# Kernel optimization log

Hardware: AMD Instinct MI355X
Metric: run time of the kernel (lower is better)

Reference implementation:

```python
import jax, jax.numpy as jnp
import numpy as np
import math

B, H, N, D = 8, 8, 2048, 64
CLIP = 10.0
NEG_INF = 1.0e10

def setup_inputs() -> dict:
    key = jax.random.key(0)
    kq, kk, kv, km = jax.random.split(key, 4)
    Q = jax.random.normal(kq, (B, H, N, D), dtype=jnp.float32)
    K = jax.random.normal(kk, (B, H, N, D), dtype=jnp.float32)
    V = jax.random.normal(kv, (B, H, N, D), dtype=jnp.float32)
    mask = jax.random.randint(km, (B, N, 1), 0, 2).astype(jnp.bool_)
    return {"Q": Q, "K": K, "V": V, "mask": mask}

def reference(Q, K, V, mask):
    scale = math.sqrt(Q.shape[-1])
    # logits: (B, H, Nq, Nk)
    logits = jnp.einsum("bhqd,bhkd->bhqk", Q, K) / scale
    logits = CLIP * jnp.tanh(logits)
    # mask (B, N, 1) -> broadcast over heads and query dim along key axis
    m = mask[:, None, None, :, 0]  # (B, 1, 1, Nk)
    logits = jnp.where(m, -NEG_INF, logits)
    probs = jax.nn.softmax(logits, axis=-1)
    return jnp.einsum("bhqk,bhkd->bhqd", probs, V)
```

## Files before the change

kernel.cpp:

```cpp
#include <hip/hip_runtime.h>

typedef __attribute__((ext_vector_type(8))) short short8;
typedef __attribute__((ext_vector_type(8))) _Float16 half8;
typedef __attribute__((ext_vector_type(2))) __fp16 fp16x2;
typedef __attribute__((ext_vector_type(2))) unsigned int uint2v;
typedef __attribute__((ext_vector_type(16))) float f32x16;
typedef __attribute__((ext_vector_type(4))) float f32x4;
typedef __attribute__((ext_vector_type(8))) unsigned short u16x8;
typedef unsigned int u32;
typedef unsigned short u16;

#define B_ 8
#define H_ 8
#define N_ 2048
#define D_ 64
#define PSTR 72
#define ELEMS 8388608
#define WS_NEED ((48ull << 20) + 4096ull)

static __device__ inline u16 bfhi(float x) {
  u32 u = __float_as_uint(x);
  return (u16)((u + 0x7FFFu + ((u >> 16) & 1u)) >> 16);
}
static __device__ inline float bf2f(u16 h) { return __uint_as_float((u32)h << 16); }
static __device__ inline u16 h2u(_Float16 h) { union { _Float16 f; u16 u; } c; c.f = h; return c.u; }

static __device__ __forceinline__ u32 pkrtz_u32(float a, float b) {
  union { fp16x2 h; u32 u; } c;
  c.h = __builtin_amdgcn_cvt_pkrtz(a, b);
  return c.u;
}

template <bool TAIL>
static __device__ __forceinline__ float pnum(float s, int key, int rem) {
  float z  = __builtin_amdgcn_exp2f(fabsf(s) * -0.36067376022224087f);
  float nu = (s >= 0.f) ? z : 1.f;
  float e  = nu * __builtin_amdgcn_rcpf(1.f + z) * -28.853900817779268f;
  if (TAIL) e = (key < rem) ? e : -16384.f;
  return __builtin_amdgcn_exp2f(e);
}

static __device__ __forceinline__ half8 pack_frag(
    float qa, float qb, float qc, float qd,
    float qe, float qf, float qg, float qh) {
  u32 E0 = pkrtz_u32(qa, qb);
  u32 E1 = pkrtz_u32(qc, qd);
  u32 O0 = pkrtz_u32(qe, qf);
  u32 O1 = pkrtz_u32(qg, qh);
  uint2v w0 = __builtin_amdgcn_permlane32_swap(E0, O0, false, false);
  uint2v w1 = __builtin_amdgcn_permlane32_swap(E1, O1, false, false);
  union { u32 u[4]; half8 v; } c;
  c.u[0] = w0[0]; c.u[1] = w1[0]; c.u[2] = w0[1]; c.u[3] = w1[1];
  return c.v;
}

struct PAFrags { half8 f0, f1, f2, f3; };

#define PN_(S, r, off) pnum<TAIL>(S[r], ((r) & 3) + 8 * ((r) >> 2) + (off), rem)
template <bool TAIL>
static __device__ __forceinline__ PAFrags softmax_repack(
    f32x16 S0, f32x16 S1, int rem) {
  PAFrags o;
  o.f0 = pack_frag(PN_(S0, 0, 0),  PN_(S0, 1, 0),  PN_(S0, 2, 0),  PN_(S0, 3, 0),
                   PN_(S0, 4, 0),  PN_(S0, 5, 0),  PN_(S0, 6, 0),  PN_(S0, 7, 0));
  o.f1 = pack_frag(PN_(S0, 8, 0),  PN_(S0, 9, 0),  PN_(S0, 10, 0), PN_(S0, 11, 0),
                   PN_(S0, 12, 0), PN_(S0, 13, 0), PN_(S0, 14, 0), PN_(S0, 15, 0));
  o.f2 = pack_frag(PN_(S1, 0, 32), PN_(S1, 1, 32), PN_(S1, 2, 32), PN_(S1, 3, 32),
                   PN_(S1, 4, 32), PN_(S1, 5, 32), PN_(S1, 6, 32), PN_(S1, 7, 32));
  o.f3 = pack_frag(PN_(S1, 8, 32), PN_(S1, 9, 32), PN_(S1, 10, 32), PN_(S1, 11, 32),
                   PN_(S1, 12, 32), PN_(S1, 13, 32), PN_(S1, 14, 32), PN_(S1, 15, 32));
  return o;
}

__global__ __launch_bounds__(256) void conv_kv2(
    const float* __restrict__ K, const float* __restrict__ V,
    const int* __restrict__ maskg,
    u16* __restrict__ Khi, u16* __restrict__ Klo, u16* __restrict__ VThi,
    int* __restrict__ cnt) {
  const int kt = blockIdx.x, bh = blockIdx.y, b = bh >> 3, tid = threadIdx.x;
  const int lane = tid & 63, wv = tid >> 6;
  __shared__ float sT[64 * 68];
  __shared__ int sIdx[64];
  __shared__ int wsum[4];
  const int n0 = tid * 8;
  u32 bits = 0; int c = 0;
#pragma unroll
  for (int i = 0; i < 8; ++i)
    if (maskg[b * N_ + n0 + i] == 0) { bits |= (1u << i); ++c; }
  int inc = c;
#pragma unroll
  for (int off = 1; off < 64; off <<= 1) {
    int v = __shfl_up(inc, off);
    if (lane >= off) inc += v;
  }
  if (lane == 63) wsum[wv] = inc;
  if (tid < 64) sIdx[tid] = -1;
  __syncthreads();
  const int cntb = wsum[0] + wsum[1] + wsum[2] + wsum[3];
  int o = inc - c;
#pragma unroll
  for (int k2 = 0; k2 < 4; ++k2) if (k2 < wv) o += wsum[k2];
  const int k0 = kt * 64;
#pragma unroll
  for (int i = 0; i < 8; ++i)
    if (bits & (1u << i)) {
      if (o >= k0 && o < k0 + 64) sIdx[o - k0] = n0 + i;
      ++o;
    }
  if (kt == 0 && (bh & 7) == 0 && tid == 0) cnt[b] = cntb;
  __syncthreads();
  const int nt = (cntb + 63) >> 6;
  if (kt >= nt) return;

  const size_t ibh = (size_t)bh * N_ * D_;
  const size_t okb = ibh + (size_t)kt * 64 * D_;
#pragma unroll
  for (int cc = 0; cc < 2; ++cc) {
    const int ci = tid + cc * 256, row = ci >> 3, seg = ci & 7;
    const int n = sIdx[row];
    f32x4 a, b2, va, vb2;
    if (n >= 0) {
      const float* kp = K + ibh + (size_t)n * D_ + seg * 8;
      a  = *(const f32x4*)kp;
      b2 = *(const f32x4*)(kp + 4);
      const float* vp = V + ibh + (size_t)n * D_ + seg * 8;
      va  = *(const f32x4*)vp;
      vb2 = *(const f32x4*)(vp + 4);
    } else {
#pragma unroll
      for (int j = 0; j < 4; ++j) { a[j] = 0.f; b2[j] = 0.f; va[j] = 0.f; vb2[j] = 0.f; }
    }
    u16x8 h, l;
#pragma unroll
    for (int j = 0; j < 4; ++j) {
      _Float16 h0 = (_Float16)a[j];
      h[j] = h2u(h0); l[j] = h2u((_Float16)(a[j] - (float)h0));
      _Float16 h1 = (_Float16)b2[j];
      h[j + 4] = h2u(h1); l[j + 4] = h2u((_Float16)(b2[j] - (float)h1));
    }
    *(u16x8*)&Khi[okb + row * D_ + seg * 8] = h;
    *(u16x8*)&Klo[okb + row * D_ + seg * 8] = l;
    *(f32x4*)&sT[row * 68 + seg * 8]     = va;
    *(f32x4*)&sT[row * 68 + seg * 8 + 4] = vb2;
  }
  __syncthreads();
  const int d = tid >> 2, ks = tid & 3;
  u16x8 h0, h1;
#pragma unroll
  for (int i = 0; i < 8; ++i) {
    h0[i] = h2u((_Float16)sT[(ks * 16 + i) * 68 + d]);
    h1[i] = h2u((_Float16)sT[(ks * 16 + i + 8) * 68 + d]);
  }
  const size_t ob = (size_t)bh * D_ * N_ + (size_t)d * N_ + (size_t)kt * 64 + ks * 16;
  *(u16x8*)&VThi[ob] = h0; *(u16x8*)&VThi[ob + 8] = h1;
}

__global__ __launch_bounds__(256, 4) void attn_mfma5(
    const float* __restrict__ Qg,
    const u16* __restrict__ Khi, const u16* __restrict__ Klo,
    const u16* __restrict__ VThi,
    const int* __restrict__ cnt, float* __restrict__ Og)
{
  const int qtile = blockIdx.x;
  const int bh = blockIdx.y, b = bh >> 3;
  const int tid = threadIdx.x, w = tid >> 6, lane = tid & 63;
  const int l32 = lane & 31, hl = lane >> 5;
  const int cntb = cnt[b];
  const int nt = (cntb + 63) >> 6;
  const bool partial = (cntb & 63) != 0;

  __shared__ short sKh[64 * PSTR], sKl[64 * PSTR];
  __shared__ short sVh[64 * PSTR];

  half8 qfh[4], qfl[4];
  {
    const float* qp = Qg + ((size_t)bh * N_ + qtile * 128 + w * 32 + l32) * D_ + hl * 8;
#pragma unroll
    for (int s = 0; s < 4; ++s) {
      f32x4 a = *(const f32x4*)(qp + s * 16);
      f32x4 c = *(const f32x4*)(qp + s * 16 + 4);
#pragma unroll
      for (int j = 0; j < 4; ++j) {
        _Float16 h0 = (_Float16)a[j];
        qfh[s][j] = h0; qfl[s][j] = (_Float16)(a[j] - (float)h0);
        _Float16 h1 = (_Float16)c[j];
        qfh[s][j + 4] = h1; qfl[s][j + 4] = (_Float16)(c[j] - (float)h1);
      }
    }
  }
  half8 ones;
#pragma unroll
  for (int j = 0; j < 8; ++j) ones[j] = (l32 == 0) ? (_Float16)1.f : (_Float16)0.f;

  f32x16 accO0, accO1, accD;
#pragma unroll
  for (int i = 0; i < 16; ++i) { accO0[i] = 0.f; accO1[i] = 0.f; accD[i] = 0.f; }

  const size_t kvb = (size_t)bh * N_ * D_;

  for (int kt = 0; kt < nt; ++kt) {
    const int k0 = kt * 64;
    __syncthreads();

#pragma unroll
    for (int cc = 0; cc < 2; ++cc) {
      const int ci = tid + cc * 256, row = ci >> 3, seg = ci & 7;
      const int lofs = row * PSTR + seg * 8;
      const size_t kofs = kvb + (size_t)(k0 + row) * D_ + seg * 8;
      *(short8*)&sKh[lofs] = *(const short8*)&Khi[kofs];
      *(short8*)&sKl[lofs] = *(const short8*)&Klo[kofs];
      const size_t vofs = kvb + (size_t)row * N_ + k0 + seg * 8;
      *(short8*)&sVh[lofs] = *(const short8*)&VThi[vofs];
    }
    __syncthreads();

    f32x16 S0, S1;
#pragma unroll
    for (int i = 0; i < 16; ++i) { S0[i] = 0.f; S1[i] = 0.f; }
    __builtin_amdgcn_s_setprio(1);
#pragma unroll
    for (int s = 0; s < 4; ++s) {
      const int o0 = l32 * PSTR + s * 16 + hl * 8;
      half8 kfh = *(const half8*)&sKh[o0];
      half8 kfl = *(const half8*)&sKl[o0];
      S0 = __builtin_amdgcn_mfma_f32_32x32x16_f16(kfh, qfh[s], S0, 0, 0, 0);
      S0 = __builtin_amdgcn_mfma_f32_32x32x16_f16(kfl, qfh[s], S0, 0, 0, 0);
      S0 = __builtin_amdgcn_mfma_f32_32x32x16_f16(kfh, qfl[s], S0, 0, 0, 0);
      const int o1 = (32 + l32) * PSTR + s * 16 + hl * 8;
      half8 kgh = *(const half8*)&sKh[o1];
      half8 kgl = *(const half8*)&sKl[o1];
      S1 = __builtin_amdgcn_mfma_f32_32x32x16_f16(kgh, qfh[s], S1, 0, 0, 0);
      S1 = __builtin_amdgcn_mfma_f32_32x32x16_f16(kgl, qfh[s], S1, 0, 0, 0);
      S1 = __builtin_amdgcn_mfma_f32_32x32x16_f16(kgh, qfl[s], S1, 0, 0, 0);
    }
    __builtin_amdgcn_s_setprio(0);

    PAFrags pa;
    if (partial && kt == nt - 1)
      pa = softmax_repack<true>(S0, S1, cntb - k0 - 4 * hl);
    else
      pa = softmax_repack<false>(S0, S1, 0);

    __builtin_amdgcn_s_setprio(1);
#pragma unroll
    for (int s = 0; s < 4; ++s) {
      half8 pf = (s == 0) ? pa.f0 : (s == 1) ? pa.f1 : (s == 2) ? pa.f2 : pa.f3;
      const int o0 = l32 * PSTR + s * 16 + hl * 8;
      half8 v0 = *(const half8*)&sVh[o0];
      accO0 = __builtin_amdgcn_mfma_f32_32x32x16_f16(pf, v0, accO0, 0, 0, 0);
      const int o1 = (32 + l32) * PSTR + s * 16 + hl * 8;
      half8 v1 = *(const half8*)&sVh[o1];
      accO1 = __builtin_amdgcn_mfma_f32_32x32x16_f16(pf, v1, accO1, 0, 0, 0);
      accD  = __builtin_amdgcn_mfma_f32_32x32x16_f16(pf, ones, accD, 0, 0, 0);
    }
    __builtin_amdgcn_s_setprio(0);
  }

  const size_t obase = (size_t)bh * N_ + qtile * 128 + w * 32;
#pragma unroll
  for (int r = 0; r < 16; ++r) {
    float den = __shfl(accD[r], lane & 32);
    float inv = (den > 0.f) ? (1.f / den) : 0.f;
    const int row = (r & 3) + 8 * (r >> 2) + 4 * hl;
    Og[(obase + row) * D_ + l32]      = accO0[r] * inv;
    Og[(obase + row) * D_ + 32 + l32] = accO1[r] * inv;
  }
}

__global__ __launch_bounds__(256, 3) void attn_mfma(
    const float* __restrict__ Qg, const float* __restrict__ Kg,
    const float* __restrict__ Vg, const int* __restrict__ maskg,
    float* __restrict__ Og)
{
  const int qtile = blockIdx.x;
  const int bh    = blockIdx.y;
  const int b     = bh >> 3;
  const int tid   = threadIdx.x;
  const int w     = tid >> 6;
  const int lane  = tid & 63;
  const int l32   = lane & 31;
  const int hl    = lane >> 5;
  const int qh    = w >> 1;
  const int kh    = w & 1;

  __shared__ short sKh[64 * PSTR], sKl[64 * PSTR];
  __shared__ short sVh[64 * PSTR], sVl[64 * PSTR];
  __shared__ short sP [64 * PSTR];
  __shared__ float sM[64];

  short8 qfh[4], qfl[4];
  {
    const float* qp = Qg + ((size_t)bh * N_ + qtile * 64 + qh * 32 + l32) * D_ + hl * 8;
#pragma unroll
    for (int s = 0; s < 4; ++s) {
      f32x4 a = *(const f32x4*)(qp + s * 16);
      f32x4 c = *(const f32x4*)(qp + s * 16 + 4);
#pragma unroll
      for (int j = 0; j < 4; ++j) {
        u16 h0 = bfhi(a[j]);
        qfh[s][j] = (short)h0;
        qfl[s][j] = (short)bfhi(a[j] - bf2f(h0));
        u16 h1 = bfhi(c[j]);
        qfh[s][j + 4] = (short)h1;
        qfl[s][j + 4] = (short)bfhi(c[j] - bf2f(h1));
      }
    }
  }
  short8 ones;
#pragma unroll
  for (int j = 0; j < 8; ++j) ones[j] = (short)((l32 == 0) ? 0x3F80 : 0);
  f32x16 accO, accD;
#pragma unroll
  for (int i = 0; i < 16; ++i) { accO[i] = 0.f; accD[i] = 0.f; }
  const size_t kvbase = (size_t)bh * N_ * D_;

  for (int kt = 0; kt < N_ / 64; ++kt) {
    const int k0 = kt * 64;
    __syncthreads();
    {
      const int row = tid >> 2, seg = tid & 3;
      const float* kp = Kg + kvbase + (size_t)(k0 + row) * D_ + seg * 16;
      short8 h0, h1, l0, l1;
#pragma unroll
      for (int i2 = 0; i2 < 2; ++i2) {
        f32x4 t0 = *(const f32x4*)(kp + i2 * 8);
        f32x4 t1 = *(const f32x4*)(kp + i2 * 8 + 4);
#pragma unroll
        for (int j = 0; j < 4; ++j) {
          u16 ha = bfhi(t0[j]); u16 la = bfhi(t0[j] - bf2f(ha));
          u16 hb = bfhi(t1[j]); u16 lb = bfhi(t1[j] - bf2f(hb));
          if (i2 == 0) { h0[j]=(short)ha; l0[j]=(short)la; h0[j+4]=(short)hb; l0[j+4]=(short)lb; }
          else         { h1[j]=(short)ha; l1[j]=(short)la; h1[j+4]=(short)hb; l1[j+4]=(short)lb; }
        }
      }
      *(short8*)&sKh[row * PSTR + seg * 16]     = h0;
      *(short8*)&sKh[row * PSTR + seg * 16 + 8] = h1;
      *(short8*)&sKl[row * PSTR + seg * 16]     = l0;
      *(short8*)&sKl[row * PSTR + seg * 16 + 8] = l1;
    }
    {
      const float* vp = Vg + kvbase + (size_t)(k0 + w * 16) * D_ + lane;
      float vv[16];
#pragma unroll
      for (int kk = 0; kk < 16; ++kk) vv[kk] = vp[(size_t)kk * D_];
      short8 h0, h1, l0, l1;
#pragma unroll
      for (int kk = 0; kk < 8; ++kk) {
        u16 ha = bfhi(vv[kk]);     h0[kk]=(short)ha; l0[kk]=(short)bfhi(vv[kk]-bf2f(ha));
        u16 hb = bfhi(vv[kk + 8]); h1[kk]=(short)hb; l1[kk]=(short)bfhi(vv[kk+8]-bf2f(hb));
      }
      *(short8*)&sVh[lane * PSTR + w * 16]     = h0;
      *(short8*)&sVh[lane * PSTR + w * 16 + 8] = h1;
      *(short8*)&sVl[lane * PSTR + w * 16]     = l0;
      *(short8*)&sVl[lane * PSTR + w * 16 + 8] = l1;
    }
    if (tid < 64) sM[tid] = maskg[b * N_ + k0 + tid] ? 0.f : 1.f;
    __syncthreads();

    f32x16 S;
#pragma unroll
    for (int i = 0; i < 16; ++i) S[i] = 0.f;
#pragma unroll
    for (int s = 0; s < 4; ++s) {
      const int off = (kh * 32 + l32) * PSTR + s * 16 + hl * 8;
      short8 kfh = *(const short8*)&sKh[off];
      short8 kfl = *(const short8*)&sKl[off];
      S = __builtin_amdgcn_mfma_f32_32x32x16_bf16(qfh[s], kfh, S, 0, 0, 0);
      S = __builtin_amdgcn_mfma_f32_32x32x16_bf16(qfl[s], kfh, S, 0, 0, 0);
      S = __builtin_amdgcn_mfma_f32_32x32x16_bf16(qfh[s], kfl, S, 0, 0, 0);
    }
    const float pm = sM[kh * 32 + l32];
#pragma unroll
    for (int r = 0; r < 16; ++r) {
      float x  = S[r] * 0.125f;
      float ax = fminf(fabsf(x), 30.f);
      float z  = __builtin_amdgcn_exp2f(ax * -2.8853900817779268f);
      float nu = (x >= 0.f) ? z : 1.f;
      float e  = nu * __builtin_amdgcn_rcpf(1.f + z) * -28.853900817779268f;
      float p  = __builtin_amdgcn_exp2f(e) * pm;
      const int row = qh * 32 + (r & 3) + 8 * (r >> 2) + 4 * hl;
      sP[row * PSTR + kh * 32 + l32] = (short)bfhi(p);
    }
    __syncthreads();
#pragma unroll
    for (int s = 0; s < 4; ++s) {
      short8 pf  = *(const short8*)&sP[(qh * 32 + l32) * PSTR + s * 16 + hl * 8];
      const int voff = (kh * 32 + l32) * PSTR + s * 16 + hl * 8;
      short8 vfh = *(const short8*)&sVh[voff];
      short8 vfl = *(const short8*)&sVl[voff];
      accO = __builtin_amdgcn_mfma_f32_32x32x16_bf16(pf, vfh, accO, 0, 0, 0);
      accO = __builtin_amdgcn_mfma_f32_32x32x16_bf16(pf, vfl, accO, 0, 0, 0);
      accD = __builtin_amdgcn_mfma_f32_32x32x16_bf16(pf, ones, accD, 0, 0, 0);
    }
  }
  const size_t obase = (size_t)bh * N_ + qtile * 64 + qh * 32;
#pragma unroll
  for (int r = 0; r < 16; ++r) {
    float den = __shfl(accD[r], lane & 32);
    float inv = (den > 0.f) ? (1.f / den) : 0.f;
    const int row = (r & 3) + 8 * (r >> 2) + 4 * hl;
    Og[(obase + row) * D_ + kh * 32 + l32] = accO[r] * inv;
  }
}

extern "C" void kernel_launch(void* const* d_in, const int* in_sizes, int n_in,
                              void* d_out, int out_size, void* d_ws, size_t ws_size,
                              hipStream_t stream) {
  const float* Q = (const float*)d_in[0];
  const float* K = (const float*)d_in[1];
  const float* V = (const float*)d_in[2];
  const int* mask = (const int*)d_in[3];
  float* out = (float*)d_out;
  dim3 block(256);
  if (ws_size >= (size_t)WS_NEED) {
    u16* wsp  = (u16*)d_ws;
    u16* Khi  = wsp;
    u16* Klo  = wsp + ELEMS;
    u16* VThi = wsp + 2 * (size_t)ELEMS;
    int* cntp = (int*)(wsp + 3 * (size_t)ELEMS);
    conv_kv2<<<dim3(32, 64), block, 0, stream>>>(K, V, mask, Khi, Klo, VThi, cntp);
    attn_mfma5<<<dim3(16, 64), block, 0, stream>>>(Q, Khi, Klo, VThi, cntp, out);
  } else {
    attn_mfma<<<dim3(32, 64), block, 0, stream>>>(Q, K, V, mask, out);
  }
}
```

Baseline: 271.5 us.

## Prefetch next KV tile into registers and replace MFMA denominator with VALU sums

The attention kernel now loads the next K/V tile from global memory into registers while the current tile's softmax and PV MFMAs run, so global latency overlaps with compute. The row-sum denominator is accumulated with scalar adds per lane plus a cross-half shuffle instead of an extra MFMA against a ones vector, removing one MFMA per step. The V transpose in the conversion kernel is rewritten to read vectorised 4x4 blocks from LDS with a different stride and to write 4-element chunks. The prefetch costs extra registers, which may affect occupancy at the 4-block launch bound.

After: 269.8 us. Within noise of the previous version (-0.6%).

```diff
diff --git a/kernel.cpp b/kernel.cpp
--- a/kernel.cpp
+++ b/kernel.cpp
@@ -6,6 +6,7 @@
 typedef __attribute__((ext_vector_type(2))) unsigned int uint2v;
 typedef __attribute__((ext_vector_type(16))) float f32x16;
 typedef __attribute__((ext_vector_type(4))) float f32x4;
+typedef __attribute__((ext_vector_type(4))) unsigned short u16x4;
 typedef __attribute__((ext_vector_type(8))) unsigned short u16x8;
 typedef unsigned int u32;
 typedef unsigned short u16;
@@ -15,6 +16,7 @@
 #define N_ 2048
 #define D_ 64
 #define PSTR 72
+#define TSTR 66
 #define ELEMS 8388608
 #define WS_NEED ((48ull << 20) + 4096ull)
 
@@ -54,32 +56,35 @@
   return c.v;
 }
 
-struct PAFrags { half8 f0, f1, f2, f3; };
-
-#define PN_(S, r, off) pnum<TAIL>(S[r], ((r) & 3) + 8 * ((r) >> 2) + (off), rem)
+struct FragSum { half8 f; float s; };
+
 template <bool TAIL>
-static __device__ __forceinline__ PAFrags softmax_repack(
-    f32x16 S0, f32x16 S1, int rem) {
-  PAFrags o;
-  o.f0 = pack_frag(PN_(S0, 0, 0),  PN_(S0, 1, 0),  PN_(S0, 2, 0),  PN_(S0, 3, 0),
-                   PN_(S0, 4, 0),  PN_(S0, 5, 0),  PN_(S0, 6, 0),  PN_(S0, 7, 0));
-  o.f1 = pack_frag(PN_(S0, 8, 0),  PN_(S0, 9, 0),  PN_(S0, 10, 0), PN_(S0, 11, 0),
-                   PN_(S0, 12, 0), PN_(S0, 13, 0), PN_(S0, 14, 0), PN_(S0, 15, 0));
-  o.f2 = pack_frag(PN_(S1, 0, 32), PN_(S1, 1, 32), PN_(S1, 2, 32), PN_(S1, 3, 32),
-                   PN_(S1, 4, 32), PN_(S1, 5, 32), PN_(S1, 6, 32), PN_(S1, 7, 32));
-  o.f3 = pack_frag(PN_(S1, 8, 32), PN_(S1, 9, 32), PN_(S1, 10, 32), PN_(S1, 11, 32),
-                   PN_(S1, 12, 32), PN_(S1, 13, 32), PN_(S1, 14, 32), PN_(S1, 15, 32));
+static __device__ __forceinline__ FragSum pack8(
+    f32x16 S, int rbase, int koff, int rem) {
+#define KEYI(i) ((((rbase) + (i)) & 3) + 8 * (((rbase) + (i)) >> 2) + (koff))
+  float pA = pnum<TAIL>(S[rbase + 0], KEYI(0), rem);
+  float pB = pnum<TAIL>(S[rbase + 1], KEYI(1), rem);
+  float pC = pnum<TAIL>(S[rbase + 2], KEYI(2), rem);
+  float pD = pnum<TAIL>(S[rbase + 3], KEYI(3), rem);
+  float pE = pnum<TAIL>(S[rbase + 4], KEYI(4), rem);
+  float pF = pnum<TAIL>(S[rbase + 5], KEYI(5), rem);
+  float pG = pnum<TAIL>(S[rbase + 6], KEYI(6), rem);
+  float pH = pnum<TAIL>(S[rbase + 7], KEYI(7), rem);
+#undef KEYI
+  FragSum o;
+  o.f = pack_frag(pA, pB, pC, pD, pE, pF, pG, pH);
+  o.s = ((pA + pB) + (pC + pD)) + ((pE + pF) + (pG + pH));
   return o;
 }
 
-__global__ __launch_bounds__(256) void conv_kv2(
+__global__ __launch_bounds__(256) void conv_kv3(
     const float* __restrict__ K, const float* __restrict__ V,
     const int* __restrict__ maskg,
     u16* __restrict__ Khi, u16* __restrict__ Klo, u16* __restrict__ VThi,
     int* __restrict__ cnt) {
   const int kt = blockIdx.x, bh = blockIdx.y, b = bh >> 3, tid = threadIdx.x;
   const int lane = tid & 63, wv = tid >> 6;
-  __shared__ float sT[64 * 68];
+  __shared__ float sT[64 * TSTR];
   __shared__ int sIdx[64];
   __shared__ int wsum[4];
   const int n0 = tid * 8;
@@ -140,22 +145,26 @@
     }
     *(u16x8*)&Khi[okb + row * D_ + seg * 8] = h;
     *(u16x8*)&Klo[okb + row * D_ + seg * 8] = l;
-    *(f32x4*)&sT[row * 68 + seg * 8]     = va;
-    *(f32x4*)&sT[row * 68 + seg * 8 + 4] = vb2;
+    *(f32x4*)&sT[row * TSTR + seg * 8]     = va;
+    *(f32x4*)&sT[row * TSTR + seg * 8 + 4] = vb2;
   }
   __syncthreads();
-  const int d = tid >> 2, ks = tid & 3;
-  u16x8 h0, h1;
-#pragma unroll
-  for (int i = 0; i < 8; ++i) {
-    h0[i] = h2u((_Float16)sT[(ks * 16 + i) * 68 + d]);
-    h1[i] = h2u((_Float16)sT[(ks * 16 + i + 8) * 68 + d]);
-  }
-  const size_t ob = (size_t)bh * D_ * N_ + (size_t)d * N_ + (size_t)kt * 64 + ks * 16;
-  *(u16x8*)&VThi[ob] = h0; *(u16x8*)&VThi[ob + 8] = h1;
-}
-
-__global__ __launch_bounds__(256, 4) void attn_mfma5(
+  const int key0 = (tid & 15) * 4, d0 = (tid >> 4) * 4;
+  f32x4 r0 = *(const f32x4*)&sT[(key0 + 0) * TSTR + d0];
+  f32x4 r1 = *(const f32x4*)&sT[(key0 + 1) * TSTR + d0];
+  f32x4 r2 = *(const f32x4*)&sT[(key0 + 2) * TSTR + d0];
+  f32x4 r3 = *(const f32x4*)&sT[(key0 + 3) * TSTR + d0];
+  const size_t ob = (size_t)bh * D_ * N_ + (size_t)kt * 64 + key0;
+#pragma unroll
+  for (int j = 0; j < 4; ++j) {
+    u16x4 ov;
+    ov[0] = h2u((_Float16)r0[j]); ov[1] = h2u((_Float16)r1[j]);
+    ov[2] = h2u((_Float16)r2[j]); ov[3] = h2u((_Float16)r3[j]);
+    *(u16x4*)&VThi[ob + (size_t)(d0 + j) * N_] = ov;
+  }
+}
+
+__global__ __launch_bounds__(256, 4) void attn_mfma6(
     const float* __restrict__ Qg,
     const u16* __restrict__ Khi, const u16* __restrict__ Klo,
     const u16* __restrict__ VThi,
@@ -188,29 +197,33 @@
       }
     }
   }
-  half8 ones;
-#pragma unroll
-  for (int j = 0; j < 8; ++j) ones[j] = (l32 == 0) ? (_Float16)1.f : (_Float16)0.f;
-
-  f32x16 accO0, accO1, accD;
-#pragma unroll
-  for (int i = 0; i < 16; ++i) { accO0[i] = 0.f; accO1[i] = 0.f; accD[i] = 0.f; }
+
+  f32x16 accO0, accO1;
+#pragma unroll
+  for (int i = 0; i < 16; ++i) { accO0[i] = 0.f; accO1[i] = 0.f; }
+  float dsum = 0.f;
 
   const size_t kvb = (size_t)bh * N_ * D_;
 
+  short8 rKh[2], rKl[2], rVh[2];
+#pragma unroll
+  for (int cc = 0; cc < 2; ++cc) {
+    const int ci = tid + cc * 256, row = ci >> 3, seg = ci & 7;
+    rKh[cc] = *(const short8*)&Khi[kvb + (size_t)row * D_ + seg * 8];
+    rKl[cc] = *(const short8*)&Klo[kvb + (size_t)row * D_ + seg * 8];
+    rVh[cc] = *(const short8*)&VThi[kvb + (size_t)row * N_ + seg * 8];
+  }
+
   for (int kt = 0; kt < nt; ++kt) {
-    const int k0 = kt * 64;
     __syncthreads();
 
 #pragma unroll
     for (int cc = 0; cc < 2; ++cc) {
       const int ci = tid + cc * 256, row = ci >> 3, seg = ci & 7;
       const int lofs = row * PSTR + seg * 8;
-      const size_t kofs = kvb + (size_t)(k0 + row) * D_ + seg * 8;
-      *(short8*)&sKh[lofs] = *(const short8*)&Khi[kofs];
-      *(short8*)&sKl[lofs] = *(const short8*)&Klo[kofs];
-      const size_t vofs = kvb + (size_t)row * N_ + k0 + seg * 8;
-      *(short8*)&sVh[lofs] = *(const short8*)&VThi[vofs];
+      *(short8*)&sKh[lofs] = rKh[cc];
+      *(short8*)&sKl[lofs] = rKl[cc];
+      *(short8*)&sVh[lofs] = rVh[cc];
     }
     __syncthreads();
 
@@ -235,33 +248,57 @@
     }
     __builtin_amdgcn_s_setprio(0);
 
-    PAFrags pa;
-    if (partial && kt == nt - 1)
-      pa = softmax_repack<true>(S0, S1, cntb - k0 - 4 * hl);
-    else
-      pa = softmax_repack<false>(S0, S1, 0);
+    FragSum fs0, fs1, fs2, fs3;
+    if (partial && kt == nt - 1) {
+      const int rem = cntb - kt * 64 - 4 * hl;
+      fs0 = pack8<true>(S0, 0, 0, rem);
+      fs1 = pack8<true>(S0, 8, 0, rem);
+      fs2 = pack8<true>(S1, 0, 32, rem);
+      fs3 = pack8<true>(S1, 8, 32, rem);
+    } else {
+      fs0 = pack8<false>(S0, 0, 0, 0);
+      fs1 = pack8<false>(S0, 8, 0, 0);
+      fs2 = pack8<false>(S1, 0, 32, 0);
+      fs3 = pack8<false>(S1, 8, 32, 0);
+    }
+    dsum += (fs0.s + fs1.s) + (fs2.s + fs3.s);
+
+    {
+      const int k0n = (kt + 1 < nt ? kt + 1 : kt) * 64;
+#pragma unroll
+      for (int cc = 0; cc < 2; ++cc) {
+        const int ci = tid + cc * 256, row = ci >> 3, seg = ci & 7;
+        rKh[cc] = *(const short8*)&Khi[kvb + (size_t)(k0n + row) * D_ + seg * 8];
+        rKl[cc] = *(const short8*)&Klo[kvb + (size_t)(k0n + row) * D_ + seg * 8];
+        rVh[cc] = *(const short8*)&VThi[kvb + (size_t)row * N_ + k0n + seg * 8];
+      }
+    }
 
     __builtin_amdgcn_s_setprio(1);
-#pragma unroll
-    for (int s = 0; s < 4; ++s) {
-      half8 pf = (s == 0) ? pa.f0 : (s == 1) ? pa.f1 : (s == 2) ? pa.f2 : pa.f3;
-      const int o0 = l32 * PSTR + s * 16 + hl * 8;
-      half8 v0 = *(const half8*)&sVh[o0];
-      accO0 = __builtin_amdgcn_mfma_f32_32x32x16_f16(pf, v0, accO0, 0, 0, 0);
-      const int o1 = (32 + l32) * PSTR + s * 16 + hl * 8;
-      half8 v1 = *(const half8*)&sVh[o1];
-      accO1 = __builtin_amdgcn_mfma_f32_32x32x16_f16(pf, v1, accO1, 0, 0, 0);
-      accD  = __builtin_amdgcn_mfma_f32_32x32x16_f16(pf, ones, accD, 0, 0, 0);
-    }
+#define PV_STEP(sI, PF)                                                        \
+    {                                                                          \
+      const int o0 = l32 * PSTR + (sI) * 16 + hl * 8;                          \
+      half8 v0 = *(const half8*)&sVh[o0];                                      \
+      accO0 = __builtin_amdgcn_mfma_f32_32x32x16_f16((PF), v0, accO0, 0, 0, 0);\
+      const int o1 = (32 + l32) * PSTR + (sI) * 16 + hl * 8;                   \
+      half8 v1 = *(const half8*)&sVh[o1];                                      \
+      accO1 = __builtin_amdgcn_mfma_f32_32x32x16_f16((PF), v1, accO1, 0, 0, 0);\
+    }
+    PV_STEP(0, fs0.f)
+    PV_STEP(1, fs1.f)
+    PV_STEP(2, fs2.f)
+    PV_STEP(3, fs3.f)
+#undef PV_STEP
     __builtin_amdgcn_s_setprio(0);
   }
 
+  float dtot = dsum + __shfl_xor(dsum, 32);
   const size_t obase = (size_t)bh * N_ + qtile * 128 + w * 32;
 #pragma unroll
   for (int r = 0; r < 16; ++r) {
-    float den = __shfl(accD[r], lane & 32);
+    const int row = (r & 3) + 8 * (r >> 2) + 4 * hl;
+    float den = __shfl(dtot, row);
     float inv = (den > 0.f) ? (1.f / den) : 0.f;
-    const int row = (r & 3) + 8 * (r >> 2) + 4 * hl;
     Og[(obase + row) * D_ + l32]      = accO0[r] * inv;
     Og[(obase + row) * D_ + 32 + l32] = accO1[r] * inv;
   }
@@ -418,8 +455,8 @@
     u16* Klo  = wsp + ELEMS;
     u16* VThi = wsp + 2 * (size_t)ELEMS;
     int* cntp = (int*)(wsp + 3 * (size_t)ELEMS);
-    conv_kv2<<<dim3(32, 64), block, 0, stream>>>(K, V, mask, Khi, Klo, VThi, cntp);
-    attn_mfma5<<<dim3(16, 64), block, 0, stream>>>(Q, Khi, Klo, VThi, cntp, out);
+    conv_kv3<<<dim3(32, 64), block, 0, stream>>>(K, V, mask, Khi, Klo, VThi, cntp);
+    attn_mfma6<<<dim3(16, 64), block, 0, stream>>>(Q, Khi, Klo, VThi, cntp, out);
   } else {
     attn_mfma<<<dim3(32, 64), block, 0, stream>>>(Q, K, V, mask, out);
   }
```
